# Optimization experiments

Measured on AMD Instinct MI355X. Metric: run time of the kernel, lower is better.

The kernel has to match this reference:

```python
import jax, jax.numpy as jnp
import numpy as np

# Dimensions: B walkers, S=2 spins, N=8 electrons/spin, D=256 features, I=4 ions
B, S, N, D, I = 8192, 2, 8, 256, 4


def setup_inputs() -> dict:
    key = jax.random.key(0)
    k1, k2, k3, k4, k5, k6 = jax.random.split(key, 6)
    eq_inputs = jax.random.normal(k1, (B, S * N, D), dtype=jnp.float32)
    r_ei = jax.random.normal(k2, (B, S * N, I, 3), dtype=jnp.float32)
    # Orbital layer params (per spin): linear kernel/bias, isotropic envelope
    W = jax.random.normal(k3, (S, D, N), dtype=jnp.float32) / np.sqrt(D)
    b = jax.random.normal(k4, (S, N), dtype=jnp.float32) * 0.1
    decay = jax.random.uniform(k5, (S, I, N), dtype=jnp.float32, minval=0.5, maxval=1.5)
    pi = jax.random.normal(k6, (S, I, N), dtype=jnp.float32)
    return {"eq_inputs": eq_inputs, "r_ei": r_ei, "W": W, "b": b, "decay": decay, "pi": pi}


def _cofactor_antieq(M):
    """M: (..., n, n) -> (..., n), i-th entry = M[i,0] * C[i,0] * (-1)**i."""
    n = M.shape[-1]
    # rows to keep when deleting row i, for each i: (n, n-1)
    full = np.arange(n)
    idx = jnp.asarray(np.stack([np.delete(full, i) for i in range(n)]))
    # delete col 0, then gather row-subsets -> (..., n, n-1, n-1)
    submats = jnp.take(M[..., 1:], idx, axis=-2)
    signs = jnp.asarray((-1.0) ** full, dtype=M.dtype)
    cof = signs * jnp.linalg.det(submats)  # (..., n)
    return M[..., 0] * cof


def reference(eq_inputs, r_ei, W, b, decay, pi):
    # split into equal spins: (B, S, N, D) and (B, S, N, I, 3)
    h = eq_inputs.reshape(B, S, N, D)
    r = r_ei.reshape(B, S, N, I, 3)
    # linear orbital part: (B, S, N, N_orb)
    lin = jnp.einsum("bsnd,sdk->bsnk", h, W) + b[:, None, :]
    # isotropic exponential envelope: sum_ion pi * exp(-decay * |r_ei|)
    dist = jnp.linalg.norm(r, axis=-1)  # (B, S, N, I)
    env = jnp.einsum("bsnik,sik->bsnk",
                     jnp.exp(-dist[..., None] * decay[:, None, :, :]), pi)
    orbitals = lin * env  # (B, S, N, N) square orbital matrices
    anti = _cofactor_antieq(orbitals)  # (B, S, N)
    out = h * anti[..., None]  # (B, S, N, D)
    return (out[:, 0], out[:, 1])
```

## Files before the change

### kernel.cpp

```cpp
#include <hip/hip_runtime.h>
#include <math.h>


__global__ __launch_bounds__(256, 8)
void orbital_cof_kernel(const float* __restrict__ h_g,
                        const float* __restrict__ r_g,
                        const float* __restrict__ W_g,
                        const float* __restrict__ b_g,
                        const float* __restrict__ dec_g,
                        const float* __restrict__ pi_g,
                        float* __restrict__ out,
                        int nb)
{
    __shared__ float hs[16][256];
    __shared__ float Ms[2][8][8];
    __shared__ float anti_s[16];
    __shared__ float dist_s[64];

    const int t = threadIdx.x;
    const int b = blockIdx.x;
    const int wave = t >> 6;
    const int lane = t & 63;
    const int s  = wave >> 1;
    const int kh = wave & 1;

    float wv[4][4];
    {
        const float* wp = W_g + s * 2048 + lane * 32 + kh * 4;
#pragma unroll
        for (int dd = 0; dd < 4; ++dd) {
            float4 w = *(const float4*)(wp + dd * 8);
            wv[dd][0] = w.x; wv[dd][1] = w.y; wv[dd][2] = w.z; wv[dd][3] = w.w;
        }
    }

    const float4* h4p = (const float4*)(h_g + (size_t)b * 4096);
    float4* hs4 = (float4*)hs;
#pragma unroll
    for (int it = 0; it < 4; ++it)
        hs4[t + it * 256] = h4p[t + it * 256];

    if (t < 64) {
        const float* rp = r_g + (size_t)b * 192 + t * 3;
        float x = rp[0], y = rp[1], z = rp[2];
        dist_s[t] = sqrtf(x * x + y * y + z * z);
    }
    __syncthreads();

    float v[32];
#pragma unroll
    for (int n = 0; n < 8; ++n) {
        float4 hv = *(const float4*)&hs[s * 8 + n][lane * 4];
#pragma unroll
        for (int kl = 0; kl < 4; ++kl) {
            float acc;
            acc = hv.x * wv[0][kl];
            acc = fmaf(hv.y, wv[1][kl], acc);
            acc = fmaf(hv.z, wv[2][kl], acc);
            acc = fmaf(hv.w, wv[3][kl], acc);
            v[n * 4 + kl] = acc;
        }
    }

#pragma unroll
    for (int i = 0; i < 16; ++i) {
        float send = (lane & 32) ? v[i] : v[i + 16];
        float recv = __shfl_xor(send, 32);
        v[i] = ((lane & 32) ? v[i + 16] : v[i]) + recv;
    }
#pragma unroll
    for (int i = 0; i < 8; ++i) {
        float send = (lane & 16) ? v[i] : v[i + 8];
        float recv = __shfl_xor(send, 16);
        v[i] = ((lane & 16) ? v[i + 8] : v[i]) + recv;
    }
#pragma unroll
    for (int i = 0; i < 4; ++i) {
        float send = (lane & 8) ? v[i] : v[i + 4];
        float recv = __shfl_xor(send, 8);
        v[i] = ((lane & 8) ? v[i + 4] : v[i]) + recv;
    }
#pragma unroll
    for (int i = 0; i < 2; ++i) {
        float send = (lane & 4) ? v[i] : v[i + 2];
        float recv = __shfl_xor(send, 4);
        v[i] = ((lane & 4) ? v[i + 2] : v[i]) + recv;
    }
    {
        float send = (lane & 2) ? v[0] : v[1];
        float recv = __shfl_xor(send, 2);
        v[0] = ((lane & 2) ? v[1] : v[0]) + recv;
    }
    float tot = v[0] + __shfl_xor(v[0], 1);

    if ((lane & 1) == 0) {
        int idx = lane >> 1;
        int n = idx >> 2;
        int k = kh * 4 + (idx & 3);
        float lin = tot + b_g[s * 8 + k];
        float env = 0.f;
#pragma unroll
        for (int i = 0; i < 4; ++i) {
            float dd = dist_s[s * 32 + n * 4 + i];
            env = fmaf(pi_g[s * 32 + i * 8 + k], __expf(-dd * dec_g[s * 32 + i * 8 + k]), env);
        }
        Ms[s][n][k] = lin * env;
    }
    __syncthreads();

    if (t < 16) {
        int ss = t >> 3;
        int n = t & 7;
        float a[7][7];
#pragma unroll
        for (int i = 0; i < 7; ++i) {
            int src = i + (i >= n);
#pragma unroll
            for (int j = 0; j < 7; ++j) a[i][j] = Ms[ss][src][j + 1];
        }
        float det = 1.f;
#pragma unroll
        for (int kk = 0; kk < 7; ++kk) {
#pragma unroll
            for (int i = kk + 1; i < 7; ++i) {
                bool sw = fabsf(a[i][kk]) > fabsf(a[kk][kk]);
#pragma unroll
                for (int j = kk; j < 7; ++j) {
                    float tk = a[kk][j], ti = a[i][j];
                    a[kk][j] = sw ? ti : tk;
                    a[i][j]  = sw ? tk : ti;
                }
                det = sw ? -det : det;
            }
            float piv = a[kk][kk];
            det *= piv;
            float rp = (piv != 0.f) ? (1.f / piv) : 0.f;
#pragma unroll
            for (int i = kk + 1; i < 7; ++i) {
                float f = a[i][kk] * rp;
#pragma unroll
                for (int j = kk + 1; j < 7; ++j) a[i][j] = fmaf(-f, a[kk][j], a[i][j]);
            }
        }
        float sgn = (n & 1) ? -1.f : 1.f;
        anti_s[t] = Ms[ss][n][0] * sgn * det;
    }
    __syncthreads();

#pragma unroll
    for (int it = 0; it < 4; ++it) {
        int f4 = t + it * 256;
        int row = f4 >> 6;
        int d4 = (f4 & 63) << 2;
        float4 hv = *(const float4*)&hs[row][d4];
        float aa = anti_s[row];
        float4 o = make_float4(hv.x * aa, hv.y * aa, hv.z * aa, hv.w * aa);
        int so = row >> 3;
        int n = row & 7;
        size_t off = (size_t)so * (size_t)nb * 2048 + (size_t)b * 2048 + (size_t)(n * 256 + d4);
        *(float4*)(out + off) = o;
    }
}

extern "C" void kernel_launch(void* const* d_in, const int* in_sizes, int n_in,
                              void* d_out, int out_size, void* d_ws, size_t ws_size,
                              hipStream_t stream) {
    int nb = in_sizes[0] / 4096;
    const float* h_g   = (const float*)d_in[0];
    const float* r_g   = (const float*)d_in[1];
    const float* W_g   = (const float*)d_in[2];
    const float* b_g   = (const float*)d_in[3];
    const float* dec_g = (const float*)d_in[4];
    const float* pi_g  = (const float*)d_in[5];
    orbital_cof_kernel<<<dim3(nb), dim3(256), 0, stream>>>(
        h_g, r_g, W_g, b_g, dec_g, pi_g, (float*)d_out, nb);
}
```

Baseline: 56.22 us.

## Make kernel persistent with register-prefetch of next walker and 512-thread blocks

Switches to a persistent grid of 768 blocks, each looping over walkers with a grid-stride loop. The next walker's h and r_ei are prefetched into registers while the current walker is processed, to hide global load latency. Blocks grow to 512 threads, so each wave computes 2 orbital columns instead of 4, which shortens the shuffle reduction. This adds an extra barrier per iteration, and the serial 16-thread determinant stage still leaves most of the block idle.

After: 82.02 us. +45.9%, slower.

```diff
diff --git a/kernel.cpp b/kernel.cpp
--- a/kernel.cpp
+++ b/kernel.cpp
@@ -2,7 +2,7 @@
 #include <math.h>
 
 
-__global__ __launch_bounds__(256, 8)
+__global__ __launch_bounds__(512, 3)
 void orbital_cof_kernel(const float* __restrict__ h_g,
                         const float* __restrict__ r_g,
                         const float* __restrict__ W_g,
@@ -18,147 +18,166 @@
     __shared__ float dist_s[64];
 
     const int t = threadIdx.x;
-    const int b = blockIdx.x;
-    const int wave = t >> 6;
-    const int lane = t & 63;
-    const int s  = wave >> 1;
-    const int kh = wave & 1;
+    const int w = t >> 6;
+    const int l = t & 63;
+    const int s  = w >> 2;
+    const int kq = w & 3;
 
-    float wv[4][4];
+    float wv[4][2];
     {
-        const float* wp = W_g + s * 2048 + lane * 32 + kh * 4;
+        const float* wp = W_g + s * 2048 + l * 32 + kq * 2;
 #pragma unroll
         for (int dd = 0; dd < 4; ++dd) {
-            float4 w = *(const float4*)(wp + dd * 8);
-            wv[dd][0] = w.x; wv[dd][1] = w.y; wv[dd][2] = w.z; wv[dd][3] = w.w;
+            float2 ww = *(const float2*)(wp + dd * 8);
+            wv[dd][0] = ww.x; wv[dd][1] = ww.y;
         }
     }
 
-    const float4* h4p = (const float4*)(h_g + (size_t)b * 4096);
-    float4* hs4 = (float4*)hs;
-#pragma unroll
-    for (int it = 0; it < 4; ++it)
-        hs4[t + it * 256] = h4p[t + it * 256];
+    const int stride = gridDim.x;
+    int b = blockIdx.x;
+    if (b >= nb) return;
 
-    if (t < 64) {
-        const float* rp = r_g + (size_t)b * 192 + t * 3;
-        float x = rp[0], y = rp[1], z = rp[2];
-        dist_s[t] = sqrtf(x * x + y * y + z * z);
-    }
-    __syncthreads();
-
-    float v[32];
-#pragma unroll
-    for (int n = 0; n < 8; ++n) {
-        float4 hv = *(const float4*)&hs[s * 8 + n][lane * 4];
-#pragma unroll
-        for (int kl = 0; kl < 4; ++kl) {
-            float acc;
-            acc = hv.x * wv[0][kl];
-            acc = fmaf(hv.y, wv[1][kl], acc);
-            acc = fmaf(hv.z, wv[2][kl], acc);
-            acc = fmaf(hv.w, wv[3][kl], acc);
-            v[n * 4 + kl] = acc;
+    float4 hr0, hr1;
+    float rx = 0.f, ry = 0.f, rz = 0.f;
+    {
+        const float4* hp = (const float4*)(h_g + (size_t)b * 4096);
+        hr0 = hp[t]; hr1 = hp[t + 512];
+        if (t < 64) {
+            const float* rp = r_g + (size_t)b * 192 + t * 3;
+            rx = rp[0]; ry = rp[1]; rz = rp[2];
         }
     }
 
+    while (true) {
+        float4* hs4 = (float4*)hs;
+        hs4[t] = hr0; hs4[t + 512] = hr1;
+        if (t < 64) dist_s[t] = sqrtf(rx * rx + ry * ry + rz * rz);
+        __syncthreads();
+
+        const int bn = b + stride;
+        if (bn < nb) {
+            const float4* hp = (const float4*)(h_g + (size_t)bn * 4096);
+            hr0 = hp[t]; hr1 = hp[t + 512];
+            if (t < 64) {
+                const float* rp = r_g + (size_t)bn * 192 + t * 3;
+                rx = rp[0]; ry = rp[1]; rz = rp[2];
+            }
+        }
+
+        float v[16];
 #pragma unroll
-    for (int i = 0; i < 16; ++i) {
-        float send = (lane & 32) ? v[i] : v[i + 16];
-        float recv = __shfl_xor(send, 32);
-        v[i] = ((lane & 32) ? v[i + 16] : v[i]) + recv;
-    }
+        for (int n = 0; n < 8; ++n) {
+            float4 hv = *(const float4*)&hs[s * 8 + n][l * 4];
 #pragma unroll
-    for (int i = 0; i < 8; ++i) {
-        float send = (lane & 16) ? v[i] : v[i + 8];
-        float recv = __shfl_xor(send, 16);
-        v[i] = ((lane & 16) ? v[i + 8] : v[i]) + recv;
-    }
+            for (int kk = 0; kk < 2; ++kk) {
+                float acc = hv.x * wv[0][kk];
+                acc = fmaf(hv.y, wv[1][kk], acc);
+                acc = fmaf(hv.z, wv[2][kk], acc);
+                acc = fmaf(hv.w, wv[3][kk], acc);
+                v[n * 2 + kk] = acc;
+            }
+        }
+
 #pragma unroll
-    for (int i = 0; i < 4; ++i) {
-        float send = (lane & 8) ? v[i] : v[i + 4];
-        float recv = __shfl_xor(send, 8);
-        v[i] = ((lane & 8) ? v[i + 4] : v[i]) + recv;
-    }
-#pragma unroll
-    for (int i = 0; i < 2; ++i) {
-        float send = (lane & 4) ? v[i] : v[i + 2];
-        float recv = __shfl_xor(send, 4);
-        v[i] = ((lane & 4) ? v[i + 2] : v[i]) + recv;
-    }
-    {
-        float send = (lane & 2) ? v[0] : v[1];
-        float recv = __shfl_xor(send, 2);
-        v[0] = ((lane & 2) ? v[1] : v[0]) + recv;
-    }
-    float tot = v[0] + __shfl_xor(v[0], 1);
-
-    if ((lane & 1) == 0) {
-        int idx = lane >> 1;
-        int n = idx >> 2;
-        int k = kh * 4 + (idx & 3);
-        float lin = tot + b_g[s * 8 + k];
-        float env = 0.f;
+        for (int i = 0; i < 8; ++i) {
+            float send = (l & 32) ? v[i] : v[i + 8];
+            float recv = __shfl_xor(send, 32);
+            v[i] = ((l & 32) ? v[i + 8] : v[i]) + recv;
+        }
 #pragma unroll
         for (int i = 0; i < 4; ++i) {
-            float dd = dist_s[s * 32 + n * 4 + i];
-            env = fmaf(pi_g[s * 32 + i * 8 + k], __expf(-dd * dec_g[s * 32 + i * 8 + k]), env);
+            float send = (l & 16) ? v[i] : v[i + 4];
+            float recv = __shfl_xor(send, 16);
+            v[i] = ((l & 16) ? v[i + 4] : v[i]) + recv;
         }
-        Ms[s][n][k] = lin * env;
-    }
-    __syncthreads();
+#pragma unroll
+        for (int i = 0; i < 2; ++i) {
+            float send = (l & 8) ? v[i] : v[i + 2];
+            float recv = __shfl_xor(send, 8);
+            v[i] = ((l & 8) ? v[i + 2] : v[i]) + recv;
+        }
+        {
+            float send = (l & 4) ? v[0] : v[1];
+            float recv = __shfl_xor(send, 4);
+            v[0] = ((l & 4) ? v[1] : v[0]) + recv;
+        }
+        float tot = v[0];
+        tot += __shfl_xor(tot, 2);
+        tot += __shfl_xor(tot, 1);
 
-    if (t < 16) {
-        int ss = t >> 3;
-        int n = t & 7;
-        float a[7][7];
+        if ((l & 3) == 0) {
+            int e = l >> 2;
+            int n = e >> 1;
+            int k = kq * 2 + (e & 1);
+            float lin = tot + b_g[s * 8 + k];
+            float env = 0.f;
 #pragma unroll
-        for (int i = 0; i < 7; ++i) {
-            int src = i + (i >= n);
+            for (int i = 0; i < 4; ++i) {
+                float dd = dist_s[s * 32 + n * 4 + i];
+                env = fmaf(pi_g[s * 32 + i * 8 + k],
+                           __expf(-dd * dec_g[s * 32 + i * 8 + k]), env);
+            }
+            Ms[s][n][k] = lin * env;
+        }
+        __syncthreads();
+
+        if (t < 16) {
+            int ss = t >> 3;
+            int n = t & 7;
+            float a[7][7];
 #pragma unroll
-            for (int j = 0; j < 7; ++j) a[i][j] = Ms[ss][src][j + 1];
+            for (int i = 0; i < 7; ++i) {
+                int src = i + (i >= n);
+#pragma unroll
+                for (int j = 0; j < 7; ++j) a[i][j] = Ms[ss][src][j + 1];
+            }
+            float det = 1.f;
+#pragma unroll
+            for (int kk = 0; kk < 7; ++kk) {
+#pragma unroll
+                for (int i = kk + 1; i < 7; ++i) {
+                    bool sw = fabsf(a[i][kk]) > fabsf(a[kk][kk]);
+#pragma unroll
+                    for (int j = kk; j < 7; ++j) {
+                        float tk = a[kk][j], ti = a[i][j];
+                        a[kk][j] = sw ? ti : tk;
+                        a[i][j]  = sw ? tk : ti;
+                    }
+                    det = sw ? -det : det;
+                }
+                float piv = a[kk][kk];
+                det *= piv;
+                float rp = (piv != 0.f) ? (1.f / piv) : 0.f;
+#pragma unroll
+                for (int i = kk + 1; i < 7; ++i) {
+                    float f = a[i][kk] * rp;
+#pragma unroll
+                    for (int j = kk + 1; j < 7; ++j) a[i][j] = fmaf(-f, a[kk][j], a[i][j]);
+                }
+            }
+            float sgn = (n & 1) ? -1.f : 1.f;
+            anti_s[t] = Ms[ss][n][0] * sgn * det;
         }
-        float det = 1.f;
-#pragma unroll
-        for (int kk = 0; kk < 7; ++kk) {
-#pragma unroll
-            for (int i = kk + 1; i < 7; ++i) {
-                bool sw = fabsf(a[i][kk]) > fabsf(a[kk][kk]);
-#pragma unroll
-                for (int j = kk; j < 7; ++j) {
-                    float tk = a[kk][j], ti = a[i][j];
-                    a[kk][j] = sw ? ti : tk;
-                    a[i][j]  = sw ? tk : ti;
-                }
-                det = sw ? -det : det;
-            }
-            float piv = a[kk][kk];
-            det *= piv;
-            float rp = (piv != 0.f) ? (1.f / piv) : 0.f;
-#pragma unroll
-            for (int i = kk + 1; i < 7; ++i) {
-                float f = a[i][kk] * rp;
-#pragma unroll
-                for (int j = kk + 1; j < 7; ++j) a[i][j] = fmaf(-f, a[kk][j], a[i][j]);
-            }
-        }
-        float sgn = (n & 1) ? -1.f : 1.f;
-        anti_s[t] = Ms[ss][n][0] * sgn * det;
-    }
-    __syncthreads();
+        __syncthreads();
 
 #pragma unroll
-    for (int it = 0; it < 4; ++it) {
-        int f4 = t + it * 256;
-        int row = f4 >> 6;
-        int d4 = (f4 & 63) << 2;
-        float4 hv = *(const float4*)&hs[row][d4];
-        float aa = anti_s[row];
-        float4 o = make_float4(hv.x * aa, hv.y * aa, hv.z * aa, hv.w * aa);
-        int so = row >> 3;
-        int n = row & 7;
-        size_t off = (size_t)so * (size_t)nb * 2048 + (size_t)b * 2048 + (size_t)(n * 256 + d4);
-        *(float4*)(out + off) = o;
+        for (int it = 0; it < 2; ++it) {
+            int f4 = t + it * 512;
+            int row = f4 >> 6;
+            int d4 = (f4 & 63) << 2;
+            float4 hv = *(const float4*)&hs[row][d4];
+            float aa = anti_s[row];
+            float4 o = make_float4(hv.x * aa, hv.y * aa, hv.z * aa, hv.w * aa);
+            int so = row >> 3;
+            int n = row & 7;
+            size_t off = (size_t)so * (size_t)nb * 2048 + (size_t)b * 2048
+                       + (size_t)(n * 256 + d4);
+            *(float4*)(out + off) = o;
+        }
+
+        if (bn >= nb) break;
+        b = bn;
+        __syncthreads();
     }
 }
 
@@ -172,6 +191,8 @@
     const float* b_g   = (const float*)d_in[3];
     const float* dec_g = (const float*)d_in[4];
     const float* pi_g  = (const float*)d_in[5];
-    orbital_cof_kernel<<<dim3(nb), dim3(256), 0, stream>>>(
+    int grid = 768;
+    if (grid > nb) grid = nb;
+    orbital_cof_kernel<<<dim3(grid), dim3(512), 0, stream>>>(
         h_g, r_g, W_g, b_g, dec_g, pi_g, (float*)d_out, nb);
 }
```
